# Optimization experiments

Measured on AMD Instinct MI355X. Metric: run time of the kernel, lower is better.

## Reference

```python
import jax, jax.numpy as jnp
import numpy as np

B, M, N, DIM, P, Q, OUT = 8, 128, 128, 3, 3, 3, 512


def setup_inputs() -> dict:
    key = jax.random.key(0)
    k1, k2, k3, k4, k5 = jax.random.split(key, 5)
    # homogeneous control points [B, m, n, dim+1]; last channel is the NURBS weight w
    ctrl_pts = jax.random.uniform(k1, (B, M, N, DIM + 1), dtype=jnp.float32)
    ctrl_pts = ctrl_pts.at[..., DIM].add(0.5)  # keep weights bounded away from 0
    # knot-span indices per (u,v) grid point: uspan in [P, M-1], vspan in [Q, N-1]
    uspan_uv = jax.random.randint(k2, (OUT, OUT), 0, M - P) + P
    vspan_uv = jax.random.randint(k3, (OUT, OUT), 0, N - Q) + Q
    # precomputed B-spline basis values [OUT, OUT, degree+1]
    Nu_uv = jax.random.uniform(k4, (OUT, OUT, P + 1), dtype=jnp.float32)
    Nv_uv = jax.random.uniform(k5, (OUT, OUT, Q + 1), dtype=jnp.float32)
    return {"ctrl_pts": ctrl_pts, "Nu_uv": Nu_uv, "Nv_uv": Nv_uv,
            "uspan_uv": uspan_uv, "vspan_uv": vspan_uv}


def reference(ctrl_pts, Nu_uv, Nv_uv, uspan_uv, vspan_uv):
    p = Nu_uv.shape[-1] - 1
    q = Nv_uv.shape[-1] - 1
    # control-point index windows: [U, V, p+1] and [U, V, q+1]
    iu = uspan_uv[..., None] - p + jnp.arange(p + 1)
    iv = vspan_uv[..., None] - q + jnp.arange(q + 1)
    # gather local (p+1)x(q+1) control-point patch per eval point:
    # [B, U, V, p+1, q+1, dim+1]
    patch = ctrl_pts[:, iu[:, :, :, None], iv[:, :, None, :], :]
    # basis-weighted sum over local patch (homogeneous coords)
    sw = jnp.einsum('buvlrc,uvl,uvr->buvc', patch, Nu_uv, Nv_uv)
    # rational (perspective) divide by weight channel
    return sw[..., :-1] / sw[..., -1:]
```

## Files before the change

### kernel.cpp

```cpp
#include <hip/hip_runtime.h>
#include <hip/hip_fp16.h>


#define OUTD 512
#define UVN  (OUTD * OUTD)
#define MD   128
#define ND   128
#define BD   8

__device__ __forceinline__ ushort4 cvt4h(const float4 c) {
    ushort4 h;
    h.x = __half_as_ushort(__float2half(c.x));
    h.y = __half_as_ushort(__float2half(c.y));
    h.z = __half_as_ushort(__float2half(c.z));
    h.w = __half_as_ushort(__float2half(c.w));
    return h;
}

__global__ __launch_bounds__(256) void transpose_h_kernel(
    const float4* __restrict__ ctrl, ushort4* __restrict__ ctrlH)
{
    const int tid = blockIdx.x * blockDim.x + threadIdx.x;
    const int b   = tid & 7;
    const int mn  = tid >> 3;
    ctrlH[tid] = cvt4h(ctrl[b * (MD * ND) + mn]);
}

__global__ __launch_bounds__(256) void surfeval_h2_kernel(
    const uint4* __restrict__ ctrlH4,
    const float4* __restrict__ Nu4,
    const float4* __restrict__ Nv4,
    const int* __restrict__ uspan,
    const int* __restrict__ vspan,
    float* __restrict__ out)
{
    __shared__ float rs[BD * 196];

    const int tidx = threadIdx.x;
    const int bp   = tidx & 3;
    const int uvL  = tidx >> 2;
    const int uv   = blockIdx.x * 64 + uvL;

    const int us3 = uspan[uv] - 3;
    const int vs3 = vspan[uv] - 3;
    const float4 nu = Nu4[uv];
    const float4 nv = Nv4[uv];
    const float nuL[4] = {nu.x, nu.y, nu.z, nu.w};
    const float nvL[4] = {nv.x, nv.y, nv.z, nv.w};

    const uint4* cp = ctrlH4 + ((size_t)(us3 * ND + vs3) * 4 + bp);

    uint4 c[4][4];
    #pragma unroll
    for (int l = 0; l < 4; ++l) {
        const uint4* row = cp + l * (ND * 4);
        #pragma unroll
        for (int r = 0; r < 4; ++r)
            c[l][r] = row[r * 4];
    }

    float ax0 = 0.f, ay0 = 0.f, az0 = 0.f, aw0 = 0.f;
    float ax1 = 0.f, ay1 = 0.f, az1 = 0.f, aw1 = 0.f;
    #pragma unroll
    for (int l = 0; l < 4; ++l) {
        #pragma unroll
        for (int r = 0; r < 4; ++r) {
            const float w = nuL[l] * nvL[r];
            const float2 a01 = __half22float2(*reinterpret_cast<const __half2*>(&c[l][r].x));
            const float2 a23 = __half22float2(*reinterpret_cast<const __half2*>(&c[l][r].y));
            const float2 b01 = __half22float2(*reinterpret_cast<const __half2*>(&c[l][r].z));
            const float2 b23 = __half22float2(*reinterpret_cast<const __half2*>(&c[l][r].w));
            ax0 = fmaf(w, a01.x, ax0); ay0 = fmaf(w, a01.y, ay0);
            az0 = fmaf(w, a23.x, az0); aw0 = fmaf(w, a23.y, aw0);
            ax1 = fmaf(w, b01.x, ax1); ay1 = fmaf(w, b01.y, ay1);
            az1 = fmaf(w, b23.x, az1); aw1 = fmaf(w, b23.y, aw1);
        }
    }

    const float inv0 = 1.0f / aw0;
    const float inv1 = 1.0f / aw1;
    const int b0 = 2 * bp;
    float* r0 = &rs[b0 * 196 + uvL * 3];
    r0[0] = ax0 * inv0; r0[1] = ay0 * inv0; r0[2] = az0 * inv0;
    float* r1 = &rs[(b0 + 1) * 196 + uvL * 3];
    r1[0] = ax1 * inv1; r1[1] = ay1 * inv1; r1[2] = az1 * inv1;

    __syncthreads();

    #pragma unroll
    for (int k = tidx; k < 384; k += 256) {
        const int b = k / 48;
        const int j = k - b * 48;
        const float4 v = *reinterpret_cast<const float4*>(&rs[b * 196 + j * 4]);
        float* dst = out + (size_t)b * (UVN * 3) + (size_t)blockIdx.x * 192 + j * 4;
        *reinterpret_cast<float4*>(dst) = v;
    }
}

__global__ __launch_bounds__(256) void surfeval_naive_kernel(
    const float* __restrict__ ctrl, const float* __restrict__ Nu,
    const float* __restrict__ Nv, const int* __restrict__ uspan,
    const int* __restrict__ vspan, float* __restrict__ out)
{
    const int tid = blockIdx.x * blockDim.x + threadIdx.x;
    const int uv = tid & (UVN - 1);
    const int b  = tid >> 18;
    const int us = uspan[uv];
    const int vs = vspan[uv];
    const float4 nu = reinterpret_cast<const float4*>(Nu)[uv];
    const float4 nv = reinterpret_cast<const float4*>(Nv)[uv];
    const float nuL[4] = {nu.x, nu.y, nu.z, nu.w};
    const float nvL[4] = {nv.x, nv.y, nv.z, nv.w};
    const float4* cp = reinterpret_cast<const float4*>(ctrl)
                     + ((b * MD + (us - 3)) * ND + (vs - 3));
    float ax = 0.f, ay = 0.f, az = 0.f, aw = 0.f;
    #pragma unroll
    for (int l = 0; l < 4; ++l) {
        const float4* row = cp + l * ND;
        #pragma unroll
        for (int r = 0; r < 4; ++r) {
            const float w = nuL[l] * nvL[r];
            const float4 cc = row[r];
            ax = fmaf(w, cc.x, ax); ay = fmaf(w, cc.y, ay);
            az = fmaf(w, cc.z, az); aw = fmaf(w, cc.w, aw);
        }
    }
    const float inv = 1.0f / aw;
    float* o = out + (size_t)tid * 3;
    o[0] = ax * inv; o[1] = ay * inv; o[2] = az * inv;
}

extern "C" void kernel_launch(void* const* d_in, const int* in_sizes, int n_in,
                              void* d_out, int out_size, void* d_ws, size_t ws_size,
                              hipStream_t stream) {
    const float* ctrl  = (const float*)d_in[0];
    const float* Nu    = (const float*)d_in[1];
    const float* Nv    = (const float*)d_in[2];
    const int*   uspan = (const int*)d_in[3];
    const int*   vspan = (const int*)d_in[4];
    float* out = (float*)d_out;

    const size_t ctrlH_bytes = (size_t)MD * ND * BD * 8;

    if (ws_size >= ctrlH_bytes) {
        ushort4* ctrlH = (ushort4*)d_ws;
        transpose_h_kernel<<<(MD * ND * BD) / 256, 256, 0, stream>>>(
            (const float4*)ctrl, ctrlH);
        surfeval_h2_kernel<<<UVN / 64, 256, 0, stream>>>(
            (const uint4*)ctrlH, (const float4*)Nu, (const float4*)Nv,
            uspan, vspan, out);
    } else {
        surfeval_naive_kernel<<<(BD * UVN) / 256, 256, 0, stream>>>(
            ctrl, Nu, Nv, uspan, vspan, out);
    }
}
```

Measured before the change: 27.52 us.

## Stage per-batch fp16 control grid in LDS and pack spans and basis to half

Adds a new path with a prep kernel that converts the control points to fp16 in per-batch layout, packs the u/v span indices into one 32-bit word and converts the basis values to fp16. The main kernel then loads a whole batch's 128x128 half-precision control grid (128 KB) into shared memory per 1024-thread block and gathers the 4x4 patches from LDS instead of global/L2. The aim is to cut scattered global gathers and reduce the bytes read for span and basis data. In exchange, each block loads the full 128 KB grid (a large LDS footprint that allows only one block per CU, with 256 blocks in total), span and basis data are reread once per batch, and output stores are strided 3-float writes. The basis values now carry fp16 rounding.

Result: slower. 29.52 us (+7.3%).

```diff
diff --git a/kernel.cpp b/kernel.cpp
--- a/kernel.cpp
+++ b/kernel.cpp
@@ -7,6 +7,11 @@
 #define MD   128
 #define ND   128
 #define BD   8
+#define MN   (MD * ND)
+#define TPB  1024
+#define NCHUNK 32
+#define UVPC (UVN / NCHUNK)
+#define ITERS (UVPC / TPB)
 
 __device__ __forceinline__ ushort4 cvt4h(const float4 c) {
     ushort4 h;
@@ -17,13 +22,102 @@
     return h;
 }
 
+__device__ __forceinline__ uint2 pack4h(const float4 c) {
+    __half2 h01 = __floats2half2_rn(c.x, c.y);
+    __half2 h23 = __floats2half2_rn(c.z, c.w);
+    uint2 u;
+    u.x = *reinterpret_cast<unsigned int*>(&h01);
+    u.y = *reinterpret_cast<unsigned int*>(&h23);
+    return u;
+}
+
+__global__ __launch_bounds__(256) void prep11_kernel(
+    const float4* __restrict__ ctrl, uint2* __restrict__ ctrlP,
+    const float4* __restrict__ Nu4, const float4* __restrict__ Nv4,
+    const int* __restrict__ uspan, const int* __restrict__ vspan,
+    unsigned int* __restrict__ spk, uint2* __restrict__ nuh, uint2* __restrict__ nvh)
+{
+    const int t = blockIdx.x * 256 + threadIdx.x;
+    if (t < BD * MN) {
+        ctrlP[t] = pack4h(ctrl[t]);
+        return;
+    }
+    const int uv = t - BD * MN;
+    spk[uv] = (unsigned int)(uspan[uv] - 3) | ((unsigned int)(vspan[uv] - 3) << 8);
+    nuh[uv] = pack4h(Nu4[uv]);
+    nvh[uv] = pack4h(Nv4[uv]);
+}
+
+__global__ __launch_bounds__(TPB) void surfeval_r11_kernel(
+    const uint2* __restrict__ ctrlP,
+    const unsigned int* __restrict__ spk,
+    const uint2* __restrict__ nuh,
+    const uint2* __restrict__ nvh,
+    float* __restrict__ out)
+{
+    __shared__ uint2 cl[MN];
+
+    const int bid  = blockIdx.x;
+    const int th   = bid >> 3;
+    const int b    = th & 7;
+    const int c    = (bid & 7) | ((th >> 3) << 3);
+    const int tid  = threadIdx.x;
+
+    const uint2* src = ctrlP + b * MN;
+    #pragma unroll
+    for (int i = 0; i < MN / TPB; ++i)
+        cl[i * TPB + tid] = src[i * TPB + tid];
+    __syncthreads();
+
+    const char* ldsb = (const char*)cl;
+
+    #pragma unroll 1
+    for (int it = 0; it < ITERS; ++it) {
+        const int uv = c * UVPC + it * TPB + tid;
+
+        const unsigned int sp = spk[uv];
+        const int us3 = sp & 0xFF;
+        const int vs3 = (sp >> 8) & 0xFF;
+        const uint2 nupk = nuh[uv];
+        const uint2 nvpk = nvh[uv];
+        const float2 nu01 = __half22float2(*(const __half2*)(&nupk.x));
+        const float2 nu23 = __half22float2(*(const __half2*)(&nupk.y));
+        const float2 nv01 = __half22float2(*(const __half2*)(&nvpk.x));
+        const float2 nv23 = __half22float2(*(const __half2*)(&nvpk.y));
+        const float nuL[4] = {nu01.x, nu01.y, nu23.x, nu23.y};
+        const float nvL[4] = {nv01.x, nv01.y, nv23.x, nv23.y};
+
+        const int base = (us3 * ND + vs3) * 8;
+        float ax = 0.f, ay = 0.f, az = 0.f, aw = 0.f;
+        #pragma unroll
+        for (int l = 0; l < 4; ++l) {
+            #pragma unroll
+            for (int r = 0; r < 4; ++r) {
+                const uint2 h = *(const uint2*)(ldsb + base + l * (ND * 8) + r * 8);
+                const float w = nuL[l] * nvL[r];
+                const float2 xy = __half22float2(*(const __half2*)(&h.x));
+                const float2 zw = __half22float2(*(const __half2*)(&h.y));
+                ax = fmaf(w, xy.x, ax);
+                ay = fmaf(w, xy.y, ay);
+                az = fmaf(w, zw.x, az);
+                aw = fmaf(w, zw.y, aw);
+            }
+        }
+        const float inv = 1.0f / aw;
+        float* o = out + ((size_t)b * UVN + uv) * 3;
+        o[0] = ax * inv;
+        o[1] = ay * inv;
+        o[2] = az * inv;
+    }
+}
+
 __global__ __launch_bounds__(256) void transpose_h_kernel(
     const float4* __restrict__ ctrl, ushort4* __restrict__ ctrlH)
 {
     const int tid = blockIdx.x * blockDim.x + threadIdx.x;
     const int b   = tid & 7;
     const int mn  = tid >> 3;
-    ctrlH[tid] = cvt4h(ctrl[b * (MD * ND) + mn]);
+    ctrlH[tid] = cvt4h(ctrl[b * MN + mn]);
 }
 
 __global__ __launch_bounds__(256) void surfeval_h2_kernel(
@@ -35,7 +129,6 @@
     float* __restrict__ out)
 {
     __shared__ float rs[BD * 196];
-
     const int tidx = threadIdx.x;
     const int bp   = tidx & 3;
     const int uvL  = tidx >> 2;
@@ -49,16 +142,13 @@
     const float nvL[4] = {nv.x, nv.y, nv.z, nv.w};
 
     const uint4* cp = ctrlH4 + ((size_t)(us3 * ND + vs3) * 4 + bp);
-
     uint4 c[4][4];
     #pragma unroll
     for (int l = 0; l < 4; ++l) {
         const uint4* row = cp + l * (ND * 4);
         #pragma unroll
-        for (int r = 0; r < 4; ++r)
-            c[l][r] = row[r * 4];
-    }
-
+        for (int r = 0; r < 4; ++r) c[l][r] = row[r * 4];
+    }
     float ax0 = 0.f, ay0 = 0.f, az0 = 0.f, aw0 = 0.f;
     float ax1 = 0.f, ay1 = 0.f, az1 = 0.f, aw1 = 0.f;
     #pragma unroll
@@ -76,7 +166,6 @@
             az1 = fmaf(w, b23.x, az1); aw1 = fmaf(w, b23.y, aw1);
         }
     }
-
     const float inv0 = 1.0f / aw0;
     const float inv1 = 1.0f / aw1;
     const int b0 = 2 * bp;
@@ -84,15 +173,13 @@
     r0[0] = ax0 * inv0; r0[1] = ay0 * inv0; r0[2] = az0 * inv0;
     float* r1 = &rs[(b0 + 1) * 196 + uvL * 3];
     r1[0] = ax1 * inv1; r1[1] = ay1 * inv1; r1[2] = az1 * inv1;
-
     __syncthreads();
-
     #pragma unroll
     for (int k = tidx; k < 384; k += 256) {
-        const int b = k / 48;
-        const int j = k - b * 48;
-        const float4 v = *reinterpret_cast<const float4*>(&rs[b * 196 + j * 4]);
-        float* dst = out + (size_t)b * (UVN * 3) + (size_t)blockIdx.x * 192 + j * 4;
+        const int bb = k / 48;
+        const int j  = k - bb * 48;
+        const float4 v = *reinterpret_cast<const float4*>(&rs[bb * 196 + j * 4]);
+        float* dst = out + (size_t)bb * (UVN * 3) + (size_t)blockIdx.x * 192 + j * 4;
         *reinterpret_cast<float4*>(dst) = v;
     }
 }
@@ -140,11 +227,27 @@
     const int*   vspan = (const int*)d_in[4];
     float* out = (float*)d_out;
 
-    const size_t ctrlH_bytes = (size_t)MD * ND * BD * 8;
-
-    if (ws_size >= ctrlH_bytes) {
+    const size_t oCtrl = 0;
+    const size_t oSpk  = (size_t)1 << 20;
+    const size_t oNuh  = (size_t)2 << 20;
+    const size_t oNvh  = (size_t)4 << 20;
+    const size_t wsReq = (size_t)6 << 20;
+
+    if (ws_size >= wsReq) {
+        char* ws = (char*)d_ws;
+        uint2*        ctrlP = (uint2*)(ws + oCtrl);
+        unsigned int* spkp  = (unsigned int*)(ws + oSpk);
+        uint2*        nuhp  = (uint2*)(ws + oNuh);
+        uint2*        nvhp  = (uint2*)(ws + oNvh);
+
+        prep11_kernel<<<(BD * MN + UVN) / 256, 256, 0, stream>>>(
+            (const float4*)ctrl, ctrlP, (const float4*)Nu, (const float4*)Nv,
+            uspan, vspan, spkp, nuhp, nvhp);
+        surfeval_r11_kernel<<<NCHUNK * BD, TPB, 0, stream>>>(
+            ctrlP, spkp, nuhp, nvhp, out);
+    } else if (ws_size >= (size_t)MN * BD * 8) {
         ushort4* ctrlH = (ushort4*)d_ws;
-        transpose_h_kernel<<<(MD * ND * BD) / 256, 256, 0, stream>>>(
+        transpose_h_kernel<<<(MN * BD) / 256, 256, 0, stream>>>(
             (const float4*)ctrl, ctrlH);
         surfeval_h2_kernel<<<UVN / 64, 256, 0, stream>>>(
             (const uint4*)ctrlH, (const float4*)Nu, (const float4*)Nv,
```
